# Optimization experiments

Measured on AMD Instinct MI355X. Metric: run time of the kernel, lower is better.

The kernel has to match this reference:

```python
import jax, jax.numpy as jnp
import numpy as np

DIM = 128  # matches init kwarg `dim`; scale = 1/sqrt(dim)


def setup_inputs() -> dict:
    key = jax.random.key(0)
    kq, kk, kv = jax.random.split(key, 3)
    B, S, D = 16, 2048, 128
    return {
        "query": jax.random.normal(kq, (B, S, D), dtype=jnp.float32),
        "key": jax.random.normal(kk, (B, S, D), dtype=jnp.float32),
        "value": jax.random.normal(kv, (B, S, D), dtype=jnp.float32),
    }


def reference(query, key, value):
    # scores = Q K^T / sqrt(dim)  -> [B, S, S]
    scale = 1.0 / np.sqrt(DIM).astype(np.float32)
    scores = jnp.einsum("bqd,bkd->bqk", query, key) * scale
    attn = jax.nn.softmax(scores, axis=-1)
    # context = attn @ V -> [B, S, D]
    return jnp.einsum("bqk,bkd->bqd", attn, value)
```

## Files before the change

### kernel.cpp

```cpp
#include <hip/hip_runtime.h>
#include <hip/hip_bf16.h>

namespace {

constexpr int kS  = 2048;
constexpr int kD  = 128;
constexpr int kKB = 128;
constexpr int kNT = kS / kKB;
constexpr int kChunks = 2048;
constexpr size_t kImgUShorts = (size_t)16 * 16 * kChunks * 8;

typedef __attribute__((ext_vector_type(8)))  short bf16x8;
typedef __attribute__((ext_vector_type(16))) float f32x16;
typedef __attribute__((ext_vector_type(4)))  unsigned int u32x4;

__device__ inline unsigned short f2bf(float f) {
  return __builtin_bit_cast(unsigned short, __float2bfloat16(f));
}
__device__ inline unsigned pk2(float lo, float hi) {
  return (unsigned)f2bf(lo) | ((unsigned)f2bf(hi) << 16);
}
__device__ inline float fexp2(float x) { return __builtin_amdgcn_exp2f(x); }

__device__ inline void gload_lds16(const void* g, void* l) {
  __builtin_amdgcn_global_load_lds(
      (const __attribute__((address_space(1))) unsigned int*)g,
      (__attribute__((address_space(3))) unsigned int*)l, 16, 0, 0);
}

__global__ __launch_bounds__(256)
void convert_kv(const float* __restrict__ K, const float* __restrict__ V,
                unsigned short* __restrict__ Kws, unsigned short* __restrict__ Vws)
{
  const int tid = threadIdx.x;
  const int gid = blockIdx.x & 255;
  const int b = gid >> 4, t = gid & 15;
  if (blockIdx.x < 256) {
    const float* src = K + ((size_t)b * kS + t * kKB) * kD;
    unsigned short* dst = Kws + (size_t)gid * kChunks * 8;
#pragma unroll
    for (int i = 0; i < 8; ++i) {
      const int CH = i * 256 + tid;
      const int k = CH >> 4, s = CH & 15;
      const int d8 = s ^ (k & 15);
      const float* p = src + (size_t)k * kD + d8 * 8;
      float4 a = *reinterpret_cast<const float4*>(p);
      float4 c = *reinterpret_cast<const float4*>(p + 4);
      bf16x8 o;
      o[0] = (short)f2bf(a.x); o[1] = (short)f2bf(a.y);
      o[2] = (short)f2bf(a.z); o[3] = (short)f2bf(a.w);
      o[4] = (short)f2bf(c.x); o[5] = (short)f2bf(c.y);
      o[6] = (short)f2bf(c.z); o[7] = (short)f2bf(c.w);
      *reinterpret_cast<bf16x8*>(dst + (size_t)CH * 8) = o;
    }
  } else {
    __shared__ unsigned short VT[128 * 136];
    const float* src = V + ((size_t)b * kS + t * kKB) * kD;
#pragma unroll
    for (int i = 0; i < 16; ++i) {
      const int idx = i * 256 + tid;
      const int k = idx >> 5, d4 = idx & 31;
      float4 v = *reinterpret_cast<const float4*>(src + (size_t)k * kD + d4 * 4);
      VT[(d4 * 4 + 0) * 136 + k] = f2bf(v.x);
      VT[(d4 * 4 + 1) * 136 + k] = f2bf(v.y);
      VT[(d4 * 4 + 2) * 136 + k] = f2bf(v.z);
      VT[(d4 * 4 + 3) * 136 + k] = f2bf(v.w);
    }
    __syncthreads();
    unsigned short* dst = Vws + (size_t)gid * kChunks * 8;
#pragma unroll
    for (int i = 0; i < 8; ++i) {
      const int CH = i * 256 + tid;
      const int d = CH >> 4, s = CH & 15;
      const int k8 = s ^ (d & 15);
      bf16x8 v = *reinterpret_cast<const bf16x8*>(&VT[d * 136 + k8 * 8]);
      *reinterpret_cast<bf16x8*>(dst + (size_t)CH * 8) = v;
    }
  }
}

__global__ __launch_bounds__(1024, 4)
void attn_fwd(const float* __restrict__ Q,
              const unsigned short* __restrict__ Kws,
              const unsigned short* __restrict__ Vws,
              float* __restrict__ O)
{
  __shared__ __align__(16) unsigned char smem[163840];

  const int tid  = threadIdx.x;
  const int wv   = tid >> 6;
  const int qg   = wv & 3;
  const int ksp  = wv >> 2;
  const int lane = tid & 63;
  const int l31  = lane & 31;
  const int hi   = lane >> 5;
  const int m15  = l31 & 15;

  const int bid   = blockIdx.x;
  const int xcd   = bid & 7;
  const int slot  = bid >> 3;
  const int batch = xcd * 2 + (slot >> 4);
  const int qtile = slot & 15;

  const float* Qb = Q + (size_t)batch * kS * kD;
  float*       Ob = O + (size_t)batch * kS * kD;

  auto stage = [&](int t, int buf) {
    const size_t base = ((size_t)(batch * 16 + t) * kChunks + wv * 128 + lane) * 8;
    unsigned char* kd = smem + buf * 32768 + wv * 2048;
    gload_lds16(Kws + base,           kd);
    gload_lds16(Kws + base + 64 * 8,  kd + 1024);
    unsigned char* vd = smem + 65536 + buf * 32768 + wv * 2048;
    gload_lds16(Vws + base,           vd);
    gload_lds16(Vws + base + 64 * 8,  vd + 1024);
  };

  stage(0, 0);

  constexpr float kQScale = 0.08838834764831845f * 1.4426950408889634f;
  {
    unsigned short* Qsm = reinterpret_cast<unsigned short*>(smem + 131072);
    const float* src = Qb + (size_t)(qtile * 128) * kD;
#pragma unroll
    for (int i = 0; i < 2; ++i) {
      const int idx = i * 1024 + tid;
      const int q = idx >> 4, s = idx & 15;
      const int d8 = s ^ (q & 15);
      const float* p = src + (size_t)q * kD + d8 * 8;
      float4 a = *reinterpret_cast<const float4*>(p);
      float4 b = *reinterpret_cast<const float4*>(p + 4);
      bf16x8 f;
      f[0] = (short)f2bf(a.x * kQScale); f[1] = (short)f2bf(a.y * kQScale);
      f[2] = (short)f2bf(a.z * kQScale); f[3] = (short)f2bf(a.w * kQScale);
      f[4] = (short)f2bf(b.x * kQScale); f[5] = (short)f2bf(b.y * kQScale);
      f[6] = (short)f2bf(b.z * kQScale); f[7] = (short)f2bf(b.w * kQScale);
      *reinterpret_cast<bf16x8*>(&Qsm[(size_t)q * 128 + s * 8]) = f;
    }
  }

  f32x16 acc[4];
#pragma unroll
  for (int dt = 0; dt < 4; ++dt)
#pragma unroll
    for (int r = 0; r < 16; ++r) acc[dt][r] = 0.f;
  float mrun = -1e30f, lrun = 0.f;

  __syncthreads();

  const unsigned short* Ksm = reinterpret_cast<const unsigned short*>(smem);
  const unsigned short* Vsm = reinterpret_cast<const unsigned short*>(smem + 65536);
  const unsigned short* Qsm = reinterpret_cast<const unsigned short*>(smem + 131072);
  const int kRowBase = (ksp * 32 + l31) * 128;
  const int qRowBase = (qg  * 32 + l31) * 128;

  for (int t = 0; t < kNT; ++t) {
    const int cur = t & 1;
    if (t + 1 < kNT) stage(t + 1, cur ^ 1);

    f32x16 sc;
#pragma unroll
    for (int r = 0; r < 16; ++r) sc[r] = 0.f;
    __builtin_amdgcn_s_setprio(1);
#pragma unroll
    for (int c = 0; c < 8; ++c) {
      const int s = ((c << 1) | hi) ^ m15;
      bf16x8 kf = *reinterpret_cast<const bf16x8*>(&Ksm[cur * 16384 + kRowBase + s * 8]);
      bf16x8 qf = *reinterpret_cast<const bf16x8*>(&Qsm[qRowBase + s * 8]);
      sc = __builtin_amdgcn_mfma_f32_32x32x16_bf16(kf, qf, sc, 0, 0, 0);
    }
    __builtin_amdgcn_s_setprio(0);

    float mt = sc[0];
#pragma unroll
    for (int r = 1; r < 16; ++r) mt = fmaxf(mt, sc[r]);
    mt = fmaxf(mt, __shfl_xor(mt, 32));
    const float growth = mt - mrun;
    if (!__all(growth <= 8.0f)) {
      const float mn = fmaxf(mrun, mt);
      const float corr = fexp2(mrun - mn);
      lrun *= corr;
#pragma unroll
      for (int dt = 0; dt < 4; ++dt)
#pragma unroll
        for (int r = 0; r < 16; ++r) acc[dt][r] *= corr;
      mrun = mn;
    }
    float rs = 0.f;
#pragma unroll
    for (int r = 0; r < 16; ++r) { sc[r] = fexp2(sc[r] - mrun); rs += sc[r]; }
    rs += __shfl_xor(rs, 32);
    lrun += rs;

    unsigned a0 = pk2(sc[0], sc[1]),   a1 = pk2(sc[2],  sc[3]);
    unsigned a2 = pk2(sc[4], sc[5]),   a3 = pk2(sc[6],  sc[7]);
    unsigned b0 = pk2(sc[8], sc[9]),   b1 = pk2(sc[10], sc[11]);
    unsigned b2 = pk2(sc[12], sc[13]), b3 = pk2(sc[14], sc[15]);
    asm("v_permlane32_swap_b32 %0, %1" : "+v"(a0), "+v"(a2));
    asm("v_permlane32_swap_b32 %0, %1" : "+v"(a1), "+v"(a3));
    asm("v_permlane32_swap_b32 %0, %1" : "+v"(b0), "+v"(b2));
    asm("v_permlane32_swap_b32 %0, %1" : "+v"(b1), "+v"(b3));
    u32x4 w0 = {a0, a1, a2, a3};
    u32x4 w1 = {b0, b1, b2, b3};
    bf16x8 pa0 = __builtin_bit_cast(bf16x8, w0);
    bf16x8 pa1 = __builtin_bit_cast(bf16x8, w1);

    const int s0 = ((ksp << 2) | hi) ^ m15;
    __builtin_amdgcn_s_setprio(1);
#pragma unroll
    for (int dt = 0; dt < 4; ++dt) {
      const int vRow = cur * 16384 + (dt * 32 + l31) * 128;
      bf16x8 vf0 = *reinterpret_cast<const bf16x8*>(&Vsm[vRow + s0 * 8]);
      acc[dt] = __builtin_amdgcn_mfma_f32_32x32x16_bf16(vf0, pa0, acc[dt], 0, 0, 0);
      bf16x8 vf1 = *reinterpret_cast<const bf16x8*>(&Vsm[vRow + (s0 ^ 2) * 8]);
      acc[dt] = __builtin_amdgcn_mfma_f32_32x32x16_bf16(vf1, pa1, acc[dt], 0, 0, 0);
    }
    __builtin_amdgcn_s_setprio(0);

    __syncthreads();
  }

  float* scr = reinterpret_cast<float*>(smem);
  float* mls = reinterpret_cast<float*>(smem + 131072);
  auto scrAt = [&](int reg, int q, int d) -> float& {
    return scr[reg * 4096 + q * 128 + (d ^ ((q & 7) << 2))];
  };
  auto mlAt  = [&](int qg_, int ksp_, int w, int q) -> float& {
    return mls[((qg_ * 4 + ksp_) * 2 + w) * 32 + q];
  };
  auto drow = [&](int r) { return (r & 3) + 8 * (r >> 2) + 4 * hi; };

  if (ksp >= 2) {
#pragma unroll
    for (int dt = 0; dt < 4; ++dt)
#pragma unroll
      for (int r = 0; r < 16; ++r)
        scrAt(qg + 4 * (ksp - 2), l31, dt * 32 + drow(r)) = acc[dt][r];
  }
  mlAt(qg, ksp, 0, l31) = mrun;
  mlAt(qg, ksp, 1, l31) = lrun;
  __syncthreads();
  if (ksp < 2) {
    const int p = ksp + 2;
    const float m2 = mlAt(qg, p, 0, l31), l2 = mlAt(qg, p, 1, l31);
    const float mm = fmaxf(mrun, m2);
    const float w1 = fexp2(mrun - mm), w2 = fexp2(m2 - mm);
#pragma unroll
    for (int dt = 0; dt < 4; ++dt)
#pragma unroll
      for (int r = 0; r < 16; ++r)
        acc[dt][r] = acc[dt][r] * w1 + scrAt(qg + 4 * (p - 2), l31, dt * 32 + drow(r)) * w2;
    lrun = lrun * w1 + l2 * w2;
    mrun = mm;
  }
  __syncthreads();
  if (ksp == 1) {
#pragma unroll
    for (int dt = 0; dt < 4; ++dt)
#pragma unroll
      for (int r = 0; r < 16; ++r)
        scrAt(qg, l31, dt * 32 + drow(r)) = acc[dt][r];
    mlAt(qg, 1, 0, l31) = mrun;
    mlAt(qg, 1, 1, l31) = lrun;
  }
  __syncthreads();
  if (ksp == 0) {
    const float m2 = mlAt(qg, 1, 0, l31), l2 = mlAt(qg, 1, 1, l31);
    const float mm = fmaxf(mrun, m2);
    const float w1 = fexp2(mrun - mm), w2 = fexp2(m2 - mm);
    const float inv = 1.0f / (lrun * w1 + l2 * w2);
#pragma unroll
    for (int dt = 0; dt < 4; ++dt)
#pragma unroll
      for (int r = 0; r < 16; ++r) {
        const int d = dt * 32 + drow(r);
        scrAt(qg, l31, d) = (acc[dt][r] * w1 + scrAt(qg, l31, d) * w2) * inv;
      }
  }
  __syncthreads();
  const int krow = tid >> 5, c4 = tid & 31;
#pragma unroll
  for (int i = 0; i < 4; ++i) {
    const int row = i * 32 + krow;
    const int q = row & 31;
    float4 val = *reinterpret_cast<const float4*>(
        &scr[(row >> 5) * 4096 + q * 128 + ((c4 * 4) ^ ((q & 7) << 2))]);
    *reinterpret_cast<float4*>(&Ob[(size_t)(qtile * 128 + row) * kD + c4 * 4]) = val;
  }
}

}

extern "C" void kernel_launch(void* const* d_in, const int* in_sizes, int n_in,
                              void* d_out, int out_size, void* d_ws, size_t ws_size,
                              hipStream_t stream) {
  const float* Q = (const float*)d_in[0];
  const float* K = (const float*)d_in[1];
  const float* V = (const float*)d_in[2];
  float* O = (float*)d_out;
  (void)in_sizes; (void)n_in; (void)out_size; (void)ws_size;

  unsigned short* Kws = (unsigned short*)d_ws;
  unsigned short* Vws = Kws + kImgUShorts;

  hipLaunchKernelGGL(convert_kv, dim3(512), dim3(256), 0, stream, K, V, Kws, Vws);
  hipLaunchKernelGGL(attn_fwd,   dim3(256), dim3(1024), 0, stream, Q, Kws, Vws, O);
}
```

Baseline: 63.52 us.

## Software-pipeline QK of next tile with PV of current tile

Restructures the attention loop so the QK^T MFMAs for tile t+1 are issued next to the PV MFMAs for tile t, letting softmax exp work overlap with matrix work. K and V staging are split so K is prefetched two tiles ahead and V one tile ahead, with the K and V double buffers offset in phase. The max reduction becomes a tree, and accumulator rescaling is deferred until after PV. This adds register pressure from holding packed probabilities across iterations, plus extra prologue and epilogue code.

Result: slower. 70.53 us (+11.0%).

```diff
diff --git a/kernel.cpp b/kernel.cpp
--- a/kernel.cpp
+++ b/kernel.cpp
@@ -105,17 +105,20 @@
   const float* Qb = Q + (size_t)batch * kS * kD;
   float*       Ob = O + (size_t)batch * kS * kD;
 
-  auto stage = [&](int t, int buf) {
+  auto stageK = [&](int t, int buf) {
     const size_t base = ((size_t)(batch * 16 + t) * kChunks + wv * 128 + lane) * 8;
     unsigned char* kd = smem + buf * 32768 + wv * 2048;
-    gload_lds16(Kws + base,           kd);
-    gload_lds16(Kws + base + 64 * 8,  kd + 1024);
+    gload_lds16(Kws + base,          kd);
+    gload_lds16(Kws + base + 64 * 8, kd + 1024);
+  };
+  auto stageV = [&](int t, int buf) {
+    const size_t base = ((size_t)(batch * 16 + t) * kChunks + wv * 128 + lane) * 8;
     unsigned char* vd = smem + 65536 + buf * 32768 + wv * 2048;
-    gload_lds16(Vws + base,           vd);
-    gload_lds16(Vws + base + 64 * 8,  vd + 1024);
-  };
-
-  stage(0, 0);
+    gload_lds16(Vws + base,          vd);
+    gload_lds16(Vws + base + 64 * 8, vd + 1024);
+  };
+
+  stageK(0, 0); stageV(0, 0); stageK(1, 1);
 
   constexpr float kQScale = 0.08838834764831845f * 1.4426950408889634f;
   {
@@ -144,6 +147,7 @@
 #pragma unroll
     for (int r = 0; r < 16; ++r) acc[dt][r] = 0.f;
   float mrun = -1e30f, lrun = 0.f;
+  bf16x8 pa0v, pa1v;
 
   __syncthreads();
 
@@ -153,10 +157,7 @@
   const int kRowBase = (ksp * 32 + l31) * 128;
   const int qRowBase = (qg  * 32 + l31) * 128;
 
-  for (int t = 0; t < kNT; ++t) {
-    const int cur = t & 1;
-    if (t + 1 < kNT) stage(t + 1, cur ^ 1);
-
+  auto qk = [&](int kb) -> f32x16 {
     f32x16 sc;
 #pragma unroll
     for (int r = 0; r < 16; ++r) sc[r] = 0.f;
@@ -164,60 +165,95 @@
 #pragma unroll
     for (int c = 0; c < 8; ++c) {
       const int s = ((c << 1) | hi) ^ m15;
-      bf16x8 kf = *reinterpret_cast<const bf16x8*>(&Ksm[cur * 16384 + kRowBase + s * 8]);
+      bf16x8 kf = *reinterpret_cast<const bf16x8*>(&Ksm[kb * 16384 + kRowBase + s * 8]);
       bf16x8 qf = *reinterpret_cast<const bf16x8*>(&Qsm[qRowBase + s * 8]);
       sc = __builtin_amdgcn_mfma_f32_32x32x16_bf16(kf, qf, sc, 0, 0, 0);
     }
     __builtin_amdgcn_s_setprio(0);
-
-    float mt = sc[0];
-#pragma unroll
-    for (int r = 1; r < 16; ++r) mt = fmaxf(mt, sc[r]);
-    mt = fmaxf(mt, __shfl_xor(mt, 32));
-    const float growth = mt - mrun;
-    if (!__all(growth <= 8.0f)) {
-      const float mn = fmaxf(mrun, mt);
-      const float corr = fexp2(mrun - mn);
-      lrun *= corr;
-#pragma unroll
-      for (int dt = 0; dt < 4; ++dt)
-#pragma unroll
-        for (int r = 0; r < 16; ++r) acc[dt][r] *= corr;
-      mrun = mn;
-    }
-    float rs = 0.f;
-#pragma unroll
-    for (int r = 0; r < 16; ++r) { sc[r] = fexp2(sc[r] - mrun); rs += sc[r]; }
-    rs += __shfl_xor(rs, 32);
-    lrun += rs;
-
-    unsigned a0 = pk2(sc[0], sc[1]),   a1 = pk2(sc[2],  sc[3]);
-    unsigned a2 = pk2(sc[4], sc[5]),   a3 = pk2(sc[6],  sc[7]);
-    unsigned b0 = pk2(sc[8], sc[9]),   b1 = pk2(sc[10], sc[11]);
-    unsigned b2 = pk2(sc[12], sc[13]), b3 = pk2(sc[14], sc[15]);
+    return sc;
+  };
+  auto treemax = [&](const f32x16& sc) {
+    float a0 = fmaxf(fmaxf(sc[0], sc[1]),  fmaxf(sc[2],  sc[3]));
+    float a1 = fmaxf(fmaxf(sc[4], sc[5]),  fmaxf(sc[6],  sc[7]));
+    float a2 = fmaxf(fmaxf(sc[8], sc[9]),  fmaxf(sc[10], sc[11]));
+    float a3 = fmaxf(fmaxf(sc[12], sc[13]), fmaxf(sc[14], sc[15]));
+    float mt = fmaxf(fmaxf(a0, a1), fmaxf(a2, a3));
+    return fmaxf(mt, __shfl_xor(mt, 32));
+  };
+  auto pv = [&](int vb) {
+    const int s0 = ((ksp << 2) | hi) ^ m15;
+    __builtin_amdgcn_s_setprio(1);
+#pragma unroll
+    for (int dt = 0; dt < 4; ++dt) {
+      const int vRow = vb * 16384 + (dt * 32 + l31) * 128;
+      bf16x8 vf0 = *reinterpret_cast<const bf16x8*>(&Vsm[vRow + s0 * 8]);
+      acc[dt] = __builtin_amdgcn_mfma_f32_32x32x16_bf16(vf0, pa0v, acc[dt], 0, 0, 0);
+      bf16x8 vf1 = *reinterpret_cast<const bf16x8*>(&Vsm[vRow + (s0 ^ 2) * 8]);
+      acc[dt] = __builtin_amdgcn_mfma_f32_32x32x16_bf16(vf1, pa1v, acc[dt], 0, 0, 0);
+    }
+    __builtin_amdgcn_s_setprio(0);
+  };
+  auto pack = [&](const f32x16& p) {
+    unsigned a0 = pk2(p[0], p[1]),   a1 = pk2(p[2],  p[3]);
+    unsigned a2 = pk2(p[4], p[5]),   a3 = pk2(p[6],  p[7]);
+    unsigned b0 = pk2(p[8], p[9]),   b1 = pk2(p[10], p[11]);
+    unsigned b2 = pk2(p[12], p[13]), b3 = pk2(p[14], p[15]);
     asm("v_permlane32_swap_b32 %0, %1" : "+v"(a0), "+v"(a2));
     asm("v_permlane32_swap_b32 %0, %1" : "+v"(a1), "+v"(a3));
     asm("v_permlane32_swap_b32 %0, %1" : "+v"(b0), "+v"(b2));
     asm("v_permlane32_swap_b32 %0, %1" : "+v"(b1), "+v"(b3));
     u32x4 w0 = {a0, a1, a2, a3};
     u32x4 w1 = {b0, b1, b2, b3};
-    bf16x8 pa0 = __builtin_bit_cast(bf16x8, w0);
-    bf16x8 pa1 = __builtin_bit_cast(bf16x8, w1);
-
-    const int s0 = ((ksp << 2) | hi) ^ m15;
-    __builtin_amdgcn_s_setprio(1);
-#pragma unroll
-    for (int dt = 0; dt < 4; ++dt) {
-      const int vRow = cur * 16384 + (dt * 32 + l31) * 128;
-      bf16x8 vf0 = *reinterpret_cast<const bf16x8*>(&Vsm[vRow + s0 * 8]);
-      acc[dt] = __builtin_amdgcn_mfma_f32_32x32x16_bf16(vf0, pa0, acc[dt], 0, 0, 0);
-      bf16x8 vf1 = *reinterpret_cast<const bf16x8*>(&Vsm[vRow + (s0 ^ 2) * 8]);
-      acc[dt] = __builtin_amdgcn_mfma_f32_32x32x16_bf16(vf1, pa1, acc[dt], 0, 0, 0);
-    }
-    __builtin_amdgcn_s_setprio(0);
+    pa0v = __builtin_bit_cast(bf16x8, w0);
+    pa1v = __builtin_bit_cast(bf16x8, w1);
+  };
+
+  {
+    f32x16 sc = qk(0);
+    const float mt = treemax(sc);
+    mrun = mt;
+    float rs = 0.f;
+#pragma unroll
+    for (int r = 0; r < 16; ++r) { sc[r] = fexp2(sc[r] - mrun); rs += sc[r]; }
+    rs += __shfl_xor(rs, 32);
+    lrun = rs;
+    pack(sc);
+  }
+  __syncthreads();
+
+  for (int t = 0; t < kNT - 1; ++t) {
+    const int kb = (t + 1) & 1, vb = t & 1;
+    if (t + 2 < kNT) stageK(t + 2, vb);
+    stageV(t + 1, kb);
+
+    f32x16 sc = qk(kb);
+    const float mt = treemax(sc);
+    const bool need = !__all(mt - mrun <= 8.0f);
+    const float mnew = need ? fmaxf(mrun, mt) : mrun;
+
+    pv(vb);
+
+    float rs = 0.f;
+#pragma unroll
+    for (int r = 0; r < 16; ++r) { sc[r] = fexp2(sc[r] - mnew); rs += sc[r]; }
+    rs += __shfl_xor(rs, 32);
+    if (need) {
+      const float corr = fexp2(mrun - mnew);
+      lrun *= corr;
+#pragma unroll
+      for (int dt = 0; dt < 4; ++dt)
+#pragma unroll
+        for (int r = 0; r < 16; ++r) acc[dt][r] *= corr;
+    }
+    lrun += rs;
+    mrun = mnew;
+    pack(sc);
 
     __syncthreads();
   }
+
+  pv((kNT - 1) & 1);
+  __syncthreads();
 
   float* scr = reinterpret_cast<float*>(smem);
   float* mls = reinterpret_cast<float*>(smem + 131072);
```
